# Performance work log

Hardware: AMD Instinct MI355X
Metric: run time of the kernel (lower is better)

## Reference

```python
import jax, jax.numpy as jnp
import numpy as np

EMBED_DIM = 1024
NUM_HEADS = 16
HEAD_DIM = EMBED_DIM // NUM_HEADS  # 64
GRID_H, GRID_W = 24, 24
BASE = 10000.0


def rope2d_cache(head_dim=HEAD_DIM, grid_h=GRID_H, grid_w=GRID_W, base=BASE):
    # "Concatenated Embeddings" 2D RoPE cache -> (cos, sin), each [grid_h*grid_w, head_dim]
    pos_dim = head_dim // 2
    inv_freq = 1.0 / (base ** (jnp.arange(0, pos_dim, 2, dtype=jnp.float32) / pos_dim))
    max_grid = max(grid_h, grid_w)
    positions = jnp.arange(max_grid, dtype=jnp.float32)
    freqs = positions[:, None] * inv_freq[None, :]            # [max_grid, pos_dim//2]
    emb_1d = jnp.concatenate([freqs, freqs], axis=-1)          # [max_grid, pos_dim]
    h_emb = jnp.broadcast_to(emb_1d[:grid_h, None, :], (grid_h, grid_w, pos_dim))
    w_emb = jnp.broadcast_to(emb_1d[None, :grid_w, :], (grid_h, grid_w, pos_dim))
    emb_2d = jnp.concatenate([h_emb, w_emb], axis=-1).reshape(-1, head_dim)
    return jnp.cos(emb_2d), jnp.sin(emb_2d)


def rotate_half(x):
    x1, x2 = jnp.split(x, 2, axis=-1)
    return jnp.concatenate([-x2, x1], axis=-1)


def setup_inputs() -> dict:
    key = jax.random.key(0)
    ks = jax.random.split(key, 9)
    B, S, E = 16, GRID_H * GRID_W + 1, EMBED_DIM
    s = 1.0 / np.sqrt(E)
    inp = {
        "hidden_states": jax.random.normal(ks[0], (B, S, E), dtype=jnp.float32),
        "Wq": jax.random.normal(ks[1], (E, E), dtype=jnp.float32) * s,
        "bq": jnp.zeros((E,), dtype=jnp.float32),
        "Wk": jax.random.normal(ks[2], (E, E), dtype=jnp.float32) * s,
        "bk": jnp.zeros((E,), dtype=jnp.float32),
        "Wv": jax.random.normal(ks[3], (E, E), dtype=jnp.float32) * s,
        "bv": jnp.zeros((E,), dtype=jnp.float32),
        "Wo": jax.random.normal(ks[4], (E, E), dtype=jnp.float32) * s,
        "bo": jnp.zeros((E,), dtype=jnp.float32),
    }
    return inp


def reference(hidden_states, Wq, bq, Wk, bk, Wv, bv, Wo, bo):
    B, S, E = hidden_states.shape
    H, D = NUM_HEADS, HEAD_DIM
    scale = D ** -0.5

    def proj(W, b):
        # torch Linear: x @ W.T + b; reshape to [B, H, S, D]
        y = jnp.einsum('bse,fe->bsf', hidden_states, W) + b
        return y.reshape(B, S, H, D).transpose(0, 2, 1, 3)

    q = proj(Wq, bq)
    k = proj(Wk, bk)
    v = proj(Wv, bv)

    cos, sin = rope2d_cache()                 # [num_patches, D]
    cos = cos[None, None, :, :]
    sin = sin[None, None, :, :]

    # CLS token at position 0 is untouched; RoPE applied to patch tokens 1:
    qp = q[:, :, 1:, :]
    kp = k[:, :, 1:, :]
    qp = qp * cos + rotate_half(qp) * sin
    kp = kp * cos + rotate_half(kp) * sin
    q = jnp.concatenate([q[:, :, :1, :], qp], axis=2)
    k = jnp.concatenate([k[:, :, :1, :], kp], axis=2)

    scores = jnp.einsum('bhqd,bhkd->bhqk', q, k) * scale   # [B,H,S,S]
    attn = jax.nn.softmax(scores, axis=-1)
    out = jnp.einsum('bhqk,bhkd->bhqd', attn, v)           # [B,H,S,D]
    out = out.transpose(0, 2, 1, 3).reshape(B, S, E)
    out = jnp.einsum('bse,fe->bsf', out, Wo) + bo
    return out
```

## Files before the change

kernel.cpp:

```cpp
#include <hip/hip_runtime.h>
#include <hip/hip_bf16.h>
#include <stdint.h>

typedef __bf16 bf16_t;
typedef __attribute__((ext_vector_type(4))) float floatx4;
typedef __attribute__((ext_vector_type(8))) __bf16 bf16x8;
typedef __attribute__((ext_vector_type(4))) __bf16 bf16x4;

#define MFMA16(a, b, c) __builtin_amdgcn_mfma_f32_16x16x32_bf16(a, b, c, 0, 0, 0)

#define GLOAD_LDS16(gsrc, ldst)                                                          \
  __builtin_amdgcn_global_load_lds((const __attribute__((address_space(1))) void*)(gsrc),\
                                   (__attribute__((address_space(3))) void*)(ldst),      \
                                   16, 0, 0)

#define BATCH 16
#define SEQ   577
#define EMB   1024
#define NH    16
#define HD    64
#define SPAD  640
#define MROWS (BATCH * SEQ)
#define MPAD  9344

#define EXP_C 0.1803368801111404f

#define OFF_H  0ULL
#define OFF_WQ 19136512ULL
#define OFF_WK 21233664ULL
#define OFF_WV 23330816ULL
#define OFF_WO 25427968ULL
#define OFF_Q  27525120ULL
#define OFF_K  48496640ULL
#define OFF_VT 69468160ULL
#define OFF_AO 90439680ULL

__global__ __launch_bounds__(256) void k_cast(
    const float4* __restrict__ hs, const float4* __restrict__ wq,
    const float4* __restrict__ wk, const float4* __restrict__ wv,
    const float4* __restrict__ wo, bf16x4* __restrict__ hb, bf16x4* __restrict__ wqb,
    bf16x4* __restrict__ wkb, bf16x4* __restrict__ wvb, bf16x4* __restrict__ wob) {
  int idx = blockIdx.x * 256 + threadIdx.x;
  const int H4 = MROWS * EMB / 4;
  const int W4 = EMB * EMB / 4;
  const float4* src;
  bf16x4* dst;
  int i;
  if (idx < H4) {
    src = hs; dst = hb; i = idx;
  } else {
    int r = idx - H4;
    int w = r / W4;
    if (w >= 4) return;
    i = r - w * W4;
    src = (w == 0) ? wq : (w == 1) ? wk : (w == 2) ? wv : wo;
    dst = (w == 0) ? wqb : (w == 1) ? wkb : (w == 2) ? wvb : wob;
  }
  float4 v = src[i];
  bf16x4 o;
  o.x = (bf16_t)v.x; o.y = (bf16_t)v.y; o.z = (bf16_t)v.z; o.w = (bf16_t)v.w;
  dst[i] = o;
}

__global__ __launch_bounds__(256, 3) void k_qkv(const bf16_t* __restrict__ A,
                                                const bf16_t* __restrict__ Wq,
                                                const bf16_t* __restrict__ Wk,
                                                const bf16_t* __restrict__ Wv,
                                                const float* __restrict__ bq,
                                                const float* __restrict__ bk,
                                                const float* __restrict__ bv,
                                                bf16_t* __restrict__ qb,
                                                bf16_t* __restrict__ kb,
                                                bf16_t* __restrict__ vtb) {
  __shared__ bf16_t As[128 * 32];
  __shared__ bf16_t Bs[3 * 64 * 32];
  const int hh = blockIdx.x;
  const int n0 = hh * 64;
  const int m0 = blockIdx.y * 128;
  const int t = threadIdx.x;
  const int wid = t >> 6, lane = t & 63, quad = lane >> 4, c = lane & 15;

  floatx4 acc[3][2][4];
#pragma unroll
  for (int z = 0; z < 3; z++)
#pragma unroll
    for (int i = 0; i < 2; i++)
#pragma unroll
      for (int j = 0; j < 4; j++) {
        floatx4 zz = {0.f, 0.f, 0.f, 0.f};
        acc[z][i][j] = zz;
      }

  for (int k0 = 0; k0 < EMB; k0 += 32) {
    __syncthreads();
#pragma unroll
    for (int i = 0; i < 2; i++) {
      int ci = i * 256 + t;
      int row = ci >> 2, off = (ci & 3) * 8;
      GLOAD_LDS16(A + (size_t)(m0 + row) * EMB + k0 + off, (char*)As + (i * 256 + wid * 64) * 16);
    }
    {
      int row = t >> 2, off = (t & 3) * 8;
      GLOAD_LDS16(Wq + (size_t)(n0 + row) * EMB + k0 + off, (char*)Bs + (wid * 64) * 16);
      GLOAD_LDS16(Wk + (size_t)(n0 + row) * EMB + k0 + off, (char*)Bs + 4096 + (wid * 64) * 16);
      GLOAD_LDS16(Wv + (size_t)(n0 + row) * EMB + k0 + off, (char*)Bs + 8192 + (wid * 64) * 16);
    }
    __syncthreads();
    bf16x8 af[2];
#pragma unroll
    for (int mi = 0; mi < 2; mi++)
      af[mi] = *(const bf16x8*)(As + (wid * 32 + mi * 16 + c) * 32 + quad * 8);
#pragma unroll
    for (int z = 0; z < 3; z++) {
      bf16x8 bfr[4];
#pragma unroll
      for (int ni = 0; ni < 4; ni++)
        bfr[ni] = *(const bf16x8*)(Bs + z * 2048 + (ni * 16 + c) * 32 + quad * 8);
#pragma unroll
      for (int mi = 0; mi < 2; mi++)
#pragma unroll
        for (int ni = 0; ni < 4; ni++) acc[z][mi][ni] = MFMA16(af[mi], bfr[ni], acc[z][mi][ni]);
    }
  }

  const float invf = exp2f(-(float)c * 0.8304820237218405f);

  for (int z = 0; z < 3; z++) {
    const float* bias = (z == 0) ? bq : (z == 1) ? bk : bv;
    float bias_v[4];
#pragma unroll
    for (int ni = 0; ni < 4; ni++) bias_v[ni] = bias[n0 + ni * 16 + c];
#pragma unroll
    for (int mi = 0; mi < 2; mi++) {
#pragma unroll
      for (int r = 0; r < 4; r++) {
        int m = m0 + wid * 32 + mi * 16 + quad * 4 + r;
        if (m >= MROWS) continue;
        int bb = m / SEQ;
        int s = m - bb * SEQ;
        if (z < 2) {
          float ch = 1.f, sh = 0.f, cw = 1.f, sw = 0.f;
          if (s > 0) {
            int p = s - 1;
            int hp = p / 24, wp = p - (p / 24) * 24;
            __sincosf((float)hp * invf, &sh, &ch);
            __sincosf((float)wp * invf, &sw, &cw);
          }
          bf16_t* dst = (z == 0) ? qb : kb;
          size_t rowoff = ((size_t)(bb * NH + hh) * SPAD + s) * HD;
#pragma unroll
          for (int ni = 0; ni < 4; ni++) {
            float val = acc[z][mi][ni][r] + bias_v[ni];
            float part = acc[z][mi][ni ^ 2][r] + bias_v[ni ^ 2];
            float rot = (ni < 2) ? -part : part;
            float cs = (ni < 2) ? ch : cw;
            float sn = (ni < 2) ? sh : sw;
            dst[rowoff + ni * 16 + c] = (bf16_t)(val * cs + rot * sn);
          }
        } else {
          size_t base = (size_t)(bb * NH + hh) * HD;
#pragma unroll
          for (int ni = 0; ni < 4; ni++) {
            float val = acc[z][mi][ni][r] + bias_v[ni];
            int d = ni * 16 + c;
            vtb[(base + d) * SPAD + s] = (bf16_t)val;
          }
        }
      }
    }
  }
}

#define PSTR 72
__global__ __launch_bounds__(256, 4) void k_attn(const bf16_t* __restrict__ qb,
                                                 const bf16_t* __restrict__ kb,
                                                 const bf16_t* __restrict__ vtb,
                                                 bf16_t* __restrict__ ao) {
  __shared__ bf16_t Ks[64 * PSTR];
  __shared__ bf16_t Vs[64 * PSTR];
  __shared__ bf16_t Ps[4 * 32 * PSTR];
  const int t = threadIdx.x, wid = t >> 6, lane = t & 63, quad = lane >> 4, c = lane & 15;
  const int hh = blockIdx.x, bb = blockIdx.y, qt = blockIdx.z;
  const size_t bh = (size_t)bb * NH + hh;
  const bf16_t* qbase = qb + bh * SPAD * HD + (size_t)qt * 128 * HD;
  const bf16_t* kbase = kb + bh * SPAD * HD;
  const bf16_t* vbase = vtb + bh * HD * SPAD;

  bf16x8 aq[2][2];
#pragma unroll
  for (int mi = 0; mi < 2; mi++)
#pragma unroll
    for (int h = 0; h < 2; h++)
      aq[mi][h] = *(const bf16x8*)(qbase + (size_t)(wid * 32 + mi * 16 + c) * HD + h * 32 + quad * 8);

  uint4 kr[2], vr[2];
#pragma unroll
  for (int j = 0; j < 2; j++) {
    int ci = j * 256 + t;
    int row = ci >> 3, off = (ci & 7) * 8;
    kr[j] = *(const uint4*)(kbase + (size_t)row * HD + off);
    vr[j] = *(const uint4*)(vbase + (size_t)row * SPAD + off);
  }

  bf16x8 ones;
#pragma unroll
  for (int i = 0; i < 8; i++) ones[i] = (bf16_t)1.0f;

  floatx4 acc_o[2][4], acc_l[2];
#pragma unroll
  for (int mi = 0; mi < 2; mi++) {
    floatx4 z = {0.f, 0.f, 0.f, 0.f};
    acc_l[mi] = z;
#pragma unroll
    for (int nd = 0; nd < 4; nd++) acc_o[mi][nd] = z;
  }

  bf16_t* Pw = Ps + wid * 32 * PSTR;

  for (int kt = 0; kt < 10; kt++) {
    __syncthreads();
#pragma unroll
    for (int j = 0; j < 2; j++) {
      int ci = j * 256 + t;
      int row = ci >> 3, off = (ci & 7) * 8;
      *(uint4*)((char*)Ks + (row * PSTR + off) * 2) = kr[j];
      *(uint4*)((char*)Vs + (row * PSTR + off) * 2) = vr[j];
    }
    __syncthreads();
    if (kt < 9) {
#pragma unroll
      for (int j = 0; j < 2; j++) {
        int ci = j * 256 + t;
        int row = ci >> 3, off = (ci & 7) * 8;
        kr[j] = *(const uint4*)(kbase + (size_t)((kt + 1) * 64 + row) * HD + off);
        vr[j] = *(const uint4*)(vbase + (size_t)row * SPAD + (kt + 1) * 64 + off);
      }
    }

    floatx4 sc[2][4];
#pragma unroll
    for (int ni = 0; ni < 4; ni++) {
      bf16x8 k0 = *(const bf16x8*)(Ks + (ni * 16 + c) * PSTR + quad * 8);
      bf16x8 k1 = *(const bf16x8*)(Ks + (ni * 16 + c) * PSTR + 32 + quad * 8);
#pragma unroll
      for (int mi = 0; mi < 2; mi++) {
        floatx4 zz = {0.f, 0.f, 0.f, 0.f};
        zz = MFMA16(aq[mi][0], k0, zz);
        zz = MFMA16(aq[mi][1], k1, zz);
        sc[mi][ni] = zz;
      }
    }
    if (kt == 9) {
#pragma unroll
      for (int ni = 0; ni < 4; ni++)
        if (ni * 16 + c >= 1)
#pragma unroll
          for (int mi = 0; mi < 2; mi++)
#pragma unroll
            for (int r = 0; r < 4; r++) sc[mi][ni][r] = -1e30f;
    }
#pragma unroll
    for (int mi = 0; mi < 2; mi++)
#pragma unroll
      for (int ni = 0; ni < 4; ni++)
#pragma unroll
        for (int r = 0; r < 4; r++) {
          float p = exp2f(sc[mi][ni][r] * EXP_C);
          Pw[(mi * 16 + quad * 4 + r) * PSTR + ni * 16 + c] = (bf16_t)p;
        }
    bf16x8 pa[2][2];
#pragma unroll
    for (int mi = 0; mi < 2; mi++)
#pragma unroll
      for (int h = 0; h < 2; h++)
        pa[mi][h] = *(const bf16x8*)(Pw + (mi * 16 + c) * PSTR + h * 32 + quad * 8);
#pragma unroll
    for (int nd = 0; nd < 4; nd++) {
      bf16x8 v0 = *(const bf16x8*)(Vs + (nd * 16 + c) * PSTR + quad * 8);
      bf16x8 v1 = *(const bf16x8*)(Vs + (nd * 16 + c) * PSTR + 32 + quad * 8);
#pragma unroll
      for (int mi = 0; mi < 2; mi++) {
        acc_o[mi][nd] = MFMA16(pa[mi][0], v0, acc_o[mi][nd]);
        acc_o[mi][nd] = MFMA16(pa[mi][1], v1, acc_o[mi][nd]);
      }
    }
#pragma unroll
    for (int mi = 0; mi < 2; mi++) {
      acc_l[mi] = MFMA16(pa[mi][0], ones, acc_l[mi]);
      acc_l[mi] = MFMA16(pa[mi][1], ones, acc_l[mi]);
    }
  }

#pragma unroll
  for (int mi = 0; mi < 2; mi++)
#pragma unroll
    for (int r = 0; r < 4; r++) {
      int q = qt * 128 + wid * 32 + mi * 16 + quad * 4 + r;
      if (q < SEQ) {
        size_t mrow = (size_t)bb * SEQ + q;
        float inv_l = 1.f / acc_l[mi][r];
#pragma unroll
        for (int nd = 0; nd < 4; nd++)
          ao[mrow * EMB + hh * HD + nd * 16 + c] = (bf16_t)(acc_o[mi][nd][r] * inv_l);
      }
    }
}

__global__ __launch_bounds__(256) void k_oproj(const bf16_t* __restrict__ A,
                                               const bf16_t* __restrict__ Wo,
                                               const float* __restrict__ bo,
                                               float* __restrict__ out) {
  __shared__ bf16_t As[128 * 32];
  __shared__ bf16_t Bs[128 * 32];
  const int n0 = blockIdx.x * 128, m0 = blockIdx.y * 128;
  const int t = threadIdx.x;
  const int wid = t >> 6, lane = t & 63, quad = lane >> 4, c = lane & 15;
  const int wr = wid >> 1, wc = wid & 1;
  floatx4 acc[4][4];
#pragma unroll
  for (int i = 0; i < 4; i++)
#pragma unroll
    for (int j = 0; j < 4; j++) {
      floatx4 z = {0.f, 0.f, 0.f, 0.f};
      acc[i][j] = z;
    }
  for (int k0 = 0; k0 < EMB; k0 += 32) {
    __syncthreads();
#pragma unroll
    for (int i = 0; i < 2; i++) {
      int ci = i * 256 + t;
      int row = ci >> 2, off = (ci & 3) * 8;
      GLOAD_LDS16(A + (size_t)(m0 + row) * EMB + k0 + off, (char*)As + (i * 256 + wid * 64) * 16);
      GLOAD_LDS16(Wo + (size_t)(n0 + row) * EMB + k0 + off, (char*)Bs + (i * 256 + wid * 64) * 16);
    }
    __syncthreads();
    bf16x8 af[4], bfr[4];
#pragma unroll
    for (int mi = 0; mi < 4; mi++)
      af[mi] = *(const bf16x8*)(As + (wr * 64 + mi * 16 + c) * 32 + quad * 8);
#pragma unroll
    for (int ni = 0; ni < 4; ni++)
      bfr[ni] = *(const bf16x8*)(Bs + (wc * 64 + ni * 16 + c) * 32 + quad * 8);
#pragma unroll
    for (int mi = 0; mi < 4; mi++)
#pragma unroll
      for (int ni = 0; ni < 4; ni++) acc[mi][ni] = MFMA16(af[mi], bfr[ni], acc[mi][ni]);
  }
  float bias_v[4];
#pragma unroll
  for (int ni = 0; ni < 4; ni++) bias_v[ni] = bo[n0 + wc * 64 + ni * 16 + c];
#pragma unroll
  for (int mi = 0; mi < 4; mi++)
#pragma unroll
    for (int r = 0; r < 4; r++) {
      int m = m0 + wr * 64 + mi * 16 + quad * 4 + r;
      if (m >= MROWS) continue;
#pragma unroll
      for (int ni = 0; ni < 4; ni++)
        out[(size_t)m * EMB + n0 + wc * 64 + ni * 16 + c] = acc[mi][ni][r] + bias_v[ni];
    }
}

extern "C" void kernel_launch(void* const* d_in, const int* in_sizes, int n_in, void* d_out,
                              int out_size, void* d_ws, size_t ws_size, hipStream_t stream) {
  const float* hs = (const float*)d_in[0];
  const float* Wq = (const float*)d_in[1];
  const float* bq = (const float*)d_in[2];
  const float* Wk = (const float*)d_in[3];
  const float* bk = (const float*)d_in[4];
  const float* Wv = (const float*)d_in[5];
  const float* bv = (const float*)d_in[6];
  const float* Wo = (const float*)d_in[7];
  const float* bo = (const float*)d_in[8];
  float* out = (float*)d_out;
  char* ws = (char*)d_ws;

  bf16_t* hb = (bf16_t*)(ws + OFF_H);
  bf16_t* wqb = (bf16_t*)(ws + OFF_WQ);
  bf16_t* wkb = (bf16_t*)(ws + OFF_WK);
  bf16_t* wvb = (bf16_t*)(ws + OFF_WV);
  bf16_t* wob = (bf16_t*)(ws + OFF_WO);
  bf16_t* qbuf = (bf16_t*)(ws + OFF_Q);
  bf16_t* kbuf = (bf16_t*)(ws + OFF_K);
  bf16_t* vtbuf = (bf16_t*)(ws + OFF_VT);
  bf16_t* aob = (bf16_t*)(ws + OFF_AO);


  k_cast<<<13328, 256, 0, stream>>>((const float4*)hs, (const float4*)Wq, (const float4*)Wk,
                                    (const float4*)Wv, (const float4*)Wo, (bf16x4*)hb,
                                    (bf16x4*)wqb, (bf16x4*)wkb, (bf16x4*)wvb, (bf16x4*)wob);

  dim3 gq(16, 73);
  k_qkv<<<gq, 256, 0, stream>>>(hb, wqb, wkb, wvb, bq, bk, bv, qbuf, kbuf, vtbuf);

  dim3 ga(16, 16, 5);
  k_attn<<<ga, 256, 0, stream>>>(qbuf, kbuf, vtbuf, aob);

  dim3 go(8, 73);
  k_oproj<<<go, 256, 0, stream>>>(aob, wob, bo, out);
}
```

Before: 331.0 us.

## Peel last single-key tile from attention loop and halve per-wave P buffer

The attention loop now runs 9 full 64-key tiles, and the lone 577th key is handled in a scalar epilogue with one small MFMA and a lane shuffle. This drops a nearly empty tenth tile that cost a full K/V load, two barriers and a full set of MFMAs. The P staging buffer is processed one 16-row block at a time and so is halved, and the occupancy hint rises from 4 to 5 blocks per CU. The per-mi reuse of the P buffer adds a serialization between the write and read of P within each wave.

Result: slower. 449.2 us (+35.7%).

```diff
diff --git a/kernel.cpp b/kernel.cpp
--- a/kernel.cpp
+++ b/kernel.cpp
@@ -172,13 +172,13 @@
 }
 
 #define PSTR 72
-__global__ __launch_bounds__(256, 4) void k_attn(const bf16_t* __restrict__ qb,
+__global__ __launch_bounds__(256, 5) void k_attn(const bf16_t* __restrict__ qb,
                                                  const bf16_t* __restrict__ kb,
                                                  const bf16_t* __restrict__ vtb,
                                                  bf16_t* __restrict__ ao) {
   __shared__ bf16_t Ks[64 * PSTR];
   __shared__ bf16_t Vs[64 * PSTR];
-  __shared__ bf16_t Ps[4 * 32 * PSTR];
+  __shared__ bf16_t Ps[4 * 16 * PSTR];
   const int t = threadIdx.x, wid = t >> 6, lane = t & 63, quad = lane >> 4, c = lane & 15;
   const int hh = blockIdx.x, bb = blockIdx.y, qt = blockIdx.z;
   const size_t bh = (size_t)bb * NH + hh;
@@ -215,9 +215,9 @@
     for (int nd = 0; nd < 4; nd++) acc_o[mi][nd] = z;
   }
 
-  bf16_t* Pw = Ps + wid * 32 * PSTR;
-
-  for (int kt = 0; kt < 10; kt++) {
+  bf16_t* Pw = Ps + wid * 16 * PSTR;
+
+  for (int kt = 0; kt < 9; kt++) {
     __syncthreads();
 #pragma unroll
     for (int j = 0; j < 2; j++) {
@@ -227,7 +227,7 @@
       *(uint4*)((char*)Vs + (row * PSTR + off) * 2) = vr[j];
     }
     __syncthreads();
-    if (kt < 9) {
+    if (kt < 8) {
 #pragma unroll
       for (int j = 0; j < 2; j++) {
         int ci = j * 256 + t;
@@ -250,44 +250,57 @@
         sc[mi][ni] = zz;
       }
     }
-    if (kt == 9) {
-#pragma unroll
-      for (int ni = 0; ni < 4; ni++)
-        if (ni * 16 + c >= 1)
-#pragma unroll
-          for (int mi = 0; mi < 2; mi++)
-#pragma unroll
-            for (int r = 0; r < 4; r++) sc[mi][ni][r] = -1e30f;
-    }
-#pragma unroll
-    for (int mi = 0; mi < 2; mi++)
+
+#pragma unroll
+    for (int mi = 0; mi < 2; mi++) {
 #pragma unroll
       for (int ni = 0; ni < 4; ni++)
 #pragma unroll
         for (int r = 0; r < 4; r++) {
           float p = exp2f(sc[mi][ni][r] * EXP_C);
-          Pw[(mi * 16 + quad * 4 + r) * PSTR + ni * 16 + c] = (bf16_t)p;
+          Pw[(quad * 4 + r) * PSTR + ni * 16 + c] = (bf16_t)p;
         }
-    bf16x8 pa[2][2];
-#pragma unroll
-    for (int mi = 0; mi < 2; mi++)
-#pragma unroll
-      for (int h = 0; h < 2; h++)
-        pa[mi][h] = *(const bf16x8*)(Pw + (mi * 16 + c) * PSTR + h * 32 + quad * 8);
-#pragma unroll
-    for (int nd = 0; nd < 4; nd++) {
-      bf16x8 v0 = *(const bf16x8*)(Vs + (nd * 16 + c) * PSTR + quad * 8);
-      bf16x8 v1 = *(const bf16x8*)(Vs + (nd * 16 + c) * PSTR + 32 + quad * 8);
-#pragma unroll
-      for (int mi = 0; mi < 2; mi++) {
-        acc_o[mi][nd] = MFMA16(pa[mi][0], v0, acc_o[mi][nd]);
-        acc_o[mi][nd] = MFMA16(pa[mi][1], v1, acc_o[mi][nd]);
-      }
-    }
+      bf16x8 pa0 = *(const bf16x8*)(Pw + c * PSTR + quad * 8);
+      bf16x8 pa1 = *(const bf16x8*)(Pw + c * PSTR + 32 + quad * 8);
+#pragma unroll
+      for (int nd = 0; nd < 4; nd++) {
+        bf16x8 v0 = *(const bf16x8*)(Vs + (nd * 16 + c) * PSTR + quad * 8);
+        bf16x8 v1 = *(const bf16x8*)(Vs + (nd * 16 + c) * PSTR + 32 + quad * 8);
+        acc_o[mi][nd] = MFMA16(pa0, v0, acc_o[mi][nd]);
+        acc_o[mi][nd] = MFMA16(pa1, v1, acc_o[mi][nd]);
+      }
+      acc_l[mi] = MFMA16(pa0, ones, acc_l[mi]);
+      acc_l[mi] = MFMA16(pa1, ones, acc_l[mi]);
+    }
+  }
+
+  {
+    bf16x8 klast[2];
+#pragma unroll
+    for (int h = 0; h < 2; h++) {
+      bf16x8 kk;
+#pragma unroll
+      for (int i = 0; i < 8; i++) kk[i] = (bf16_t)0.0f;
+      if (c == 0) kk = *(const bf16x8*)(kbase + (size_t)576 * HD + h * 32 + quad * 8);
+      klast[h] = kk;
+    }
+    float vlast[4];
+#pragma unroll
+    for (int nd = 0; nd < 4; nd++)
+      vlast[nd] = (float)vbase[(size_t)(nd * 16 + c) * SPAD + 576];
 #pragma unroll
     for (int mi = 0; mi < 2; mi++) {
-      acc_l[mi] = MFMA16(pa[mi][0], ones, acc_l[mi]);
-      acc_l[mi] = MFMA16(pa[mi][1], ones, acc_l[mi]);
+      floatx4 zz = {0.f, 0.f, 0.f, 0.f};
+      zz = MFMA16(aq[mi][0], klast[0], zz);
+      zz = MFMA16(aq[mi][1], klast[1], zz);
+#pragma unroll
+      for (int r = 0; r < 4; r++) {
+        float p = exp2f(zz[r] * EXP_C);
+        p = __shfl(p, quad * 16, 64);
+#pragma unroll
+        for (int nd = 0; nd < 4; nd++) acc_o[mi][nd][r] += p * vlast[nd];
+        acc_l[mi][r] += p;
+      }
     }
   }
 
```
